# Kernel optimization log

Measured on AMD Instinct MI355X. Metric: run time of the kernel, lower is better.

## Reference

```python
import jax, jax.numpy as jnp
import numpy as np

N, E, FD, PD, C0, C1 = 50000, 1000000, 1024, 64, 64, 64


def setup_inputs() -> dict:
    key = jax.random.key(0)
    ks = iter(jax.random.split(key, 64))
    nrm = lambda s, sc=0.05: jax.random.normal(next(ks), s, jnp.float32) * sc

    def bn_p(c):
        # rows: gamma, beta, running_mean, running_var (eval-mode batchnorm)
        return jnp.stack([
            1.0 + 0.1 * jax.random.normal(next(ks), (c,)),
            0.1 * jax.random.normal(next(ks), (c,)),
            0.1 * jax.random.normal(next(ks), (c,)),
            0.5 + jax.random.uniform(next(ks), (c,)),
        ]).astype(jnp.float32)

    inp = {}
    inp["x"] = jax.random.normal(next(ks), (N, FD + 4), jnp.float32)
    inp["edge_index"] = jax.random.randint(next(ks), (2, E), 0, N, jnp.int32)
    inp["edge_attr"] = jax.random.randint(next(ks), (E,), 0, 3, jnp.int32) - 1  # {-1,0,1}
    inp["Wspf"] = nrm((PD, 4)); inp["bspf"] = nrm((PD,))
    inp["W011"] = nrm((C0, FD // 2 + PD)); inp["b011"] = nrm((C0,))
    inp["W012"] = nrm((C0, FD // 2)); inp["b012"] = nrm((C0,))
    inp["bn01"] = bn_p(C0)
    for i in (1, 2, 3):
        inp[f"e{i}W1"] = nrm((C0, 2 * C0)); inp[f"e{i}b1"] = nrm((C0,))
        inp[f"e{i}W2"] = nrm((C0, C0)); inp[f"e{i}b2"] = nrm((C0,))
        inp[f"bn1{i}"] = bn_p(C0)
    inp["s21Wl"] = nrm((C1, C0)); inp["s21bl"] = nrm((C1,)); inp["s21Wr"] = nrm((C1, C0))
    inp["bn21"] = bn_p(C1)
    for i in (1, 2, 3):
        inp[f"s3{i}Wl"] = nrm((1, C1)); inp[f"s3{i}bl"] = nrm((1,)); inp[f"s3{i}Wr"] = nrm((1, C1))
    return inp


def _bn(h, p):
    g, b, m, v = p
    return (h - m) * jax.lax.rsqrt(v + 1e-5) * g + b


def _edge_conv(h, src, dst, seg, n, W1, b1, W2, b2):
    # EdgeConv: max_j MLP([x_i, x_j - x_i]); masked edges routed to dummy segment n
    xi, xj = h[dst], h[src]
    msg = jax.nn.relu(jnp.concatenate([xi, xj - xi], axis=1) @ W1.T + b1) @ W2.T + b2
    out = jax.ops.segment_max(msg, seg, num_segments=n + 1)[:n]
    return jnp.where(jnp.isfinite(out), out, 0.0)  # nodes with no in-edges -> 0


def _sage(h, src, seg, n, Wl, bl, Wr):
    # SAGEConv: lin_l(mean_j x_j) + lin_r(x_i)
    s = jax.ops.segment_sum(h[src], seg, num_segments=n + 1)[:n]
    cnt = jax.ops.segment_sum(jnp.ones((seg.shape[0],), h.dtype), seg, num_segments=n + 1)[:n]
    agg = s / jnp.maximum(cnt, 1.0)[:, None]
    return agg @ Wl.T + bl + h @ Wr.T


def reference(x, edge_index, edge_attr, Wspf, bspf, W011, b011, W012, b012, bn01,
              e1W1, e1b1, e1W2, e1b2, bn11, e2W1, e2b1, e2W2, e2b2, bn12,
              e3W1, e3b1, e3W2, e3b2, bn13, s21Wl, s21bl, s21Wr, bn21,
              s31Wl, s31bl, s31Wr, s32Wl, s32bl, s32Wr, s33Wl, s33bl, s33Wr):
    fd = 1024
    n = x.shape[0]
    src, dst = edge_index[0], edge_index[1]
    seg1 = jnp.where(edge_attr >= 0, dst, n)  # forward-time edges
    seg2 = jnp.where(edge_attr <= 0, dst, n)  # backward-time edges
    seg3 = dst                                 # all edges

    spf = x[:, fd:fd + 4]
    x_vis = jnp.concatenate([x[:, fd // 2:fd], spf @ Wspf.T + bspf], axis=1) @ W011.T + b011
    x_aud = x[:, :fd // 2] @ W012.T + b012
    h = jax.nn.relu(_bn(x_aud + x_vis, bn01))

    def branch(eW1, eb1, eW2, eb2, bnE, seg, sWl, sbl, sWr):
        y = jax.nn.relu(_bn(_edge_conv(h, src, dst, seg, n, eW1, eb1, eW2, eb2), bnE))
        y = jax.nn.relu(_bn(_sage(y, src, seg, n, s21Wl, s21bl, s21Wr), bn21))
        return _sage(y, src, seg, n, sWl, sbl, sWr)

    o = (branch(e1W1, e1b1, e1W2, e1b2, bn11, seg1, s31Wl, s31bl, s31Wr)
         + branch(e2W1, e2b1, e2W2, e2b2, bn12, seg2, s32Wl, s32bl, s32Wr)
         + branch(e3W1, e3b1, e3W2, e3b2, bn13, seg3, s33Wl, s33bl, s33Wr))
    return jax.nn.sigmoid(o)
```

## Files before the change

kernel.cpp:

```cpp
#include <hip/hip_runtime.h>
#include <cstdint>
#include <cstddef>

#define NN 50000
#define EE 1000000
#define NBK 196
#define PW_EC 6144
#define PW_AG 8192

typedef __attribute__((ext_vector_type(8))) short bf16x8;
typedef __attribute__((ext_vector_type(4))) short s16x4;
typedef __attribute__((ext_vector_type(4))) float f32x4;
typedef _Float16 f16;
typedef __attribute__((ext_vector_type(2))) _Float16 f16x2;
typedef __attribute__((ext_vector_type(4))) _Float16 f16x4;
typedef __attribute__((ext_vector_type(8))) _Float16 f16x8;

__device__ __forceinline__ void split2(float v, short& hi, short& lo) {
    union { float f; unsigned int u; } a; a.f = v;
    unsigned short h16 = (unsigned short)(a.u >> 16);
    union { unsigned int u; float f; } hf; hf.u = ((unsigned int)h16) << 16;
    union { float f; unsigned int u; } b; b.f = v - hf.f;
    hi = (short)h16;
    lo = (short)(b.u >> 16);
}

__device__ __forceinline__ f16x8 relupq(f16x8 p, f16x8 q) {
    f16x8 s = p + q;
    f16x8 z = {};
#if __has_builtin(__builtin_elementwise_max)
    return __builtin_elementwise_max(s, z);
#else
    f16x8 r;
#pragma unroll
    for (int j = 0; j < 8; j++) r[j] = (s[j] > (f16)0.f) ? s[j] : (f16)0.f;
    return r;
#endif
}

#define OFF_WHL    ((size_t)0)
#define OFF_WSPP   ((size_t)262144)
#define OFF_BIAS01 ((size_t)263168)
#define OFF_W1PQT  ((size_t)263424)
#define OFF_BIASPQ ((size_t)361728)
#define OFF_WSAGET ((size_t)363264)
#define OFF_BIAS21 ((size_t)396032)
#define OFF_BNF    ((size_t)396288)
#define OFF_W2BF   ((size_t)398848)
#define OFF_INVC4  ((size_t)423424)
#define OFF_PZ4    ((size_t)1223424)
#define OFF_RP     ((size_t)2023424)
#define OFF_PARTS  ((size_t)2223488)
#define OFF_DEG    ((size_t)2227584)
#define OFF_GHEAD  ((size_t)2427648)
#define OFF_SORT   ((size_t)2431744)
#define OFF_H      ((size_t)6431744)
#define OFF_PI     ((size_t)19231744)
#define OFF_QI     ((size_t)38431744)
#define OFF_Y1I    ((size_t)57631744)
#define OFF_EBUCK  OFF_H
#define OFF_AGGI   OFF_PI

__global__ __launch_bounds__(256) void k_prep(
    const float* __restrict__ Wspf, const float* __restrict__ bspf,
    const float* __restrict__ W011, const float* __restrict__ b011,
    const float* __restrict__ W012, const float* __restrict__ b012,
    const float* __restrict__ bn01,
    const float* __restrict__ e1W1, const float* __restrict__ e1b1,
    const float* __restrict__ e1b2, const float* __restrict__ bn11,
    const float* __restrict__ e2W1, const float* __restrict__ e2b1,
    const float* __restrict__ e2b2, const float* __restrict__ bn12,
    const float* __restrict__ e3W1, const float* __restrict__ e3b1,
    const float* __restrict__ e3b2, const float* __restrict__ bn13,
    const float* __restrict__ e1W2, const float* __restrict__ e2W2,
    const float* __restrict__ e3W2,
    const float* __restrict__ s21Wl, const float* __restrict__ s21bl,
    const float* __restrict__ s21Wr, const float* __restrict__ bn21,
    unsigned short* __restrict__ Whl, float* __restrict__ WspP, float* __restrict__ bias01,
    float* __restrict__ W1pqT, float* __restrict__ biasPQ,
    float* __restrict__ WsageT, float* __restrict__ bias21, float* __restrict__ bnf,
    f16* __restrict__ W2h)
{
    int idx = blockIdx.x * 256 + threadIdx.x;
    if (idx < 131072) {
        int hl = idx >> 16;
        int r = idx & 65535;
        int kchunk = r >> 11;
        int r2 = r & 2047;
        int blk = r2 >> 9;
        int r3 = r2 & 511;
        int lane = r3 >> 3;
        int j = r3 & 7;
        int n = lane & 15, quad = lane >> 4;
        int k = kchunk * 32 + quad * 8 + j;
        int c = blk * 16 + n;
        float s = bn01[c] * rsqrtf(bn01[192 + c] + 1e-5f);
        float w = ((k < 512) ? W012[c * 512 + k] : W011[c * 576 + (k - 512)]) * s;
        short hi, lo;
        split2(w, hi, lo);
        Whl[idx] = (unsigned short)(hl ? lo : hi);
    } else if (idx < 131072 + 24576) {
        int r = idx - 131072;
        int b = r >> 13; r &= 8191;
        int k = r >> 7, cp = r & 127;
        const float* W1 = (b == 0) ? e1W1 : (b == 1) ? e2W1 : e3W1;
        float val;
        if (cp < 64) val = W1[cp * 128 + k] - W1[cp * 128 + 64 + k];
        else         val = W1[(cp - 64) * 128 + 64 + k];
        W1pqT[b * 8192 + k * 128 + cp] = val;
    } else if (idx < 131072 + 24576 + 8192) {
        int r = idx - (131072 + 24576);
        int k = r >> 6, c = r & 63;
        float s = bn21[c] * rsqrtf(bn21[192 + c] + 1e-5f);
        float w = (k < 64) ? s21Wl[c * 64 + k] : s21Wr[c * 64 + (k - 64)];
        WsageT[k * 64 + c] = w * s;
    } else if (idx < 131072 + 24576 + 8192 + 64) {
        int c = idx - (131072 + 24576 + 8192);
        float s01 = bn01[c] * rsqrtf(bn01[192 + c] + 1e-5f);
        float wsp0 = 0.f, wsp1 = 0.f, wsp2 = 0.f, wsp3 = 0.f, bacc = 0.f;
        for (int j = 0; j < 64; j++) {
            float w = W011[c * 576 + 512 + j];
            wsp0 += w * Wspf[j * 4 + 0];
            wsp1 += w * Wspf[j * 4 + 1];
            wsp2 += w * Wspf[j * 4 + 2];
            wsp3 += w * Wspf[j * 4 + 3];
            bacc += w * bspf[j];
        }
        WspP[c * 4 + 0] = wsp0 * s01; WspP[c * 4 + 1] = wsp1 * s01;
        WspP[c * 4 + 2] = wsp2 * s01; WspP[c * 4 + 3] = wsp3 * s01;
        bias01[c] = (b011[c] + b012[c] + bacc) * s01 + (bn01[64 + c] - bn01[128 + c] * s01);
        float s21 = bn21[c] * rsqrtf(bn21[192 + c] + 1e-5f);
        bias21[c] = s21bl[c] * s21 + (bn21[64 + c] - bn21[128 + c] * s21);
        const float* b1a[3] = { e1b1, e2b1, e3b1 };
        const float* b2a[3] = { e1b2, e2b2, e3b2 };
        const float* bna[3] = { bn11, bn12, bn13 };
#pragma unroll
        for (int b = 0; b < 3; b++) {
            float s = bna[b][c] * rsqrtf(bna[b][192 + c] + 1e-5f);
            float tr = bna[b][64 + c] - bna[b][128 + c] * s;
            bnf[b * 192 + c] = s;
            bnf[b * 192 + 64 + c] = b2a[b][c] * s + tr;
            bnf[b * 192 + 128 + c] = tr;
            biasPQ[b * 128 + c] = b1a[b][c];
            biasPQ[b * 128 + 64 + c] = 0.f;
        }
    } else if (idx < 131072 + 24576 + 8192 + 64 + 12288) {
        int r = idx - (131072 + 24576 + 8192 + 64);
        int b = r >> 12, i = r & 4095;
        const float* W2 = (b == 0) ? e1W2 : (b == 1) ? e2W2 : e3W2;
        W2h[b * 4096 + i] = (f16)W2[i];
    }
}

__global__ __launch_bounds__(256) void k_hist(
    const int* __restrict__ dst, int* __restrict__ deg)
{
    int e = blockIdx.x * 256 + threadIdx.x;
    if (e < EE) atomicAdd(&deg[dst[e]], 1);
}

__global__ __launch_bounds__(256) void k_psum(const int* __restrict__ deg, int* __restrict__ parts)
{
    int i = blockIdx.x * 256 + threadIdx.x;
    int v = (i < NN) ? deg[i] : 0;
#pragma unroll
    for (int off = 32; off > 0; off >>= 1) v += __shfl_xor(v, off);
    __shared__ int ws4[4];
    int wid = threadIdx.x >> 6;
    if ((threadIdx.x & 63) == 0) ws4[wid] = v;
    __syncthreads();
    if (threadIdx.x == 0)
        parts[blockIdx.x] = ws4[0] + ws4[1] + ws4[2] + ws4[3];
}

__global__ __launch_bounds__(256) void k_pscan(int* __restrict__ parts, int* __restrict__ ghead)
{
    __shared__ int sbuf[256];
    int tid = threadIdx.x;
    int v = (tid < NBK) ? parts[tid] : 0;
    sbuf[tid] = v;
    __syncthreads();
    for (int off = 1; off < 256; off <<= 1) {
        int t = (tid >= off) ? sbuf[tid - off] : 0;
        __syncthreads();
        sbuf[tid] += t;
        __syncthreads();
    }
    if (tid < NBK) {
        int ex = sbuf[tid] - v;
        parts[tid] = ex;
        ghead[tid] = ex;
    }
}

__global__ __launch_bounds__(256) void k_scanfix(
    const int* __restrict__ deg, const int* __restrict__ parts, int* __restrict__ rowptr)
{
    __shared__ int sbuf[256];
    int tid = threadIdx.x;
    int i = blockIdx.x * 256 + tid;
    int v = (i < NN) ? deg[i] : 0;
    sbuf[tid] = v;
    __syncthreads();
    for (int off = 1; off < 256; off <<= 1) {
        int t = (tid >= off) ? sbuf[tid - off] : 0;
        __syncthreads();
        sbuf[tid] += t;
        __syncthreads();
    }
    int base = parts[blockIdx.x];
    if (i < NN)      rowptr[i] = base + sbuf[tid] - v;
    if (i == NN - 1) rowptr[NN] = base + sbuf[tid];
}

__global__ __launch_bounds__(256) void k_bucketA(
    const int* __restrict__ src, const int* __restrict__ dst, const int* __restrict__ attr,
    int* __restrict__ ghead, unsigned int* __restrict__ ebuck)
{
    __shared__ int hist[NBK];
    __shared__ int head[NBK];
    int tid = threadIdx.x;
    if (tid < NBK) hist[tid] = 0;
    __syncthreads();
    int base_e = blockIdx.x * 4096;
    unsigned int word[16]; int bkt[16];
#pragma unroll
    for (int k = 0; k < 16; k++) {
        int e = base_e + k * 256 + tid;
        if (e < EE) {
            int d = dst[e], s = src[e], a = attr[e] + 1;
            int b = d >> 8;
            word[k] = (unsigned)s | ((unsigned)a << 16) | ((unsigned)(d & 255) << 18);
            bkt[k] = b;
            atomicAdd(&hist[b], 1);
        } else { bkt[k] = -1; word[k] = 0; }
    }
    __syncthreads();
    if (tid < NBK) {
        int c = hist[tid];
        head[tid] = c ? atomicAdd(&ghead[tid], c) : 0;
    }
    __syncthreads();
#pragma unroll
    for (int k = 0; k < 16; k++) {
        if (bkt[k] >= 0) {
            int pos = atomicAdd(&head[bkt[k]], 1);
            ebuck[pos] = word[k];
        }
    }
}

__global__ __launch_bounds__(256) void k_bucketB(
    const int* __restrict__ rp, const unsigned int* __restrict__ ebuck,
    int* __restrict__ sorted)
{
    __shared__ int sbuf[256];
    __shared__ int head[256];
    int b = blockIdx.x, tid = threadIdx.x;
    int n0 = b * 256;
    int n1 = n0 + 256; if (n1 > NN) n1 = NN;
    int r0 = rp[n0];
    int r1 = rp[n1];
    sbuf[tid] = 0;
    __syncthreads();
    for (int e = r0 + tid; e < r1; e += 256)
        atomicAdd(&sbuf[(ebuck[e] >> 18) & 255], 1);
    __syncthreads();
    int v = sbuf[tid];
    for (int off = 1; off < 256; off <<= 1) {
        int t = (tid >= off) ? sbuf[tid - off] : 0;
        __syncthreads();
        sbuf[tid] += t;
        __syncthreads();
    }
    head[tid] = r0 + sbuf[tid] - v;
    __syncthreads();
    for (int e = r0 + tid; e < r1; e += 256) {
        unsigned int w = ebuck[e];
        int pos = atomicAdd(&head[(w >> 18) & 255], 1);
        sorted[pos] = (int)(w & 0x3FFFFu);
    }
}

__global__ __launch_bounds__(256) void k_h(
    const float* __restrict__ x, const unsigned short* __restrict__ Whl,
    const float* __restrict__ WspP, const float* __restrict__ bias01,
    float* __restrict__ h)
{
    __shared__ unsigned short hib[2][4096];
    __shared__ unsigned short lob[2][4096];
    int tid = threadIdx.x;
    int w = tid >> 6, l = tid & 63;
    int tile = blockIdx.x;
    int m = l & 15, quad = l >> 4;
    int blk = w;
    const unsigned short* Wh = Whl;
    const unsigned short* Wl = Whl + 65536;
    const size_t xbase = (size_t)tile * 16 * 1028;

    int oct_w = l >> 1, off_w = (l & 1) * 4;

    f32x4 g[4];
#pragma unroll
    for (int p = 0; p < 4; p++)
        g[p] = *(const f32x4*)(x + xbase + (size_t)(p * 4 + w) * 1028 + l * 4);
#pragma unroll
    for (int p = 0; p < 4; p++) {
        int r = p * 4 + w;
        int op = r * 256 + (oct_w ^ (r & 7)) * 8 + off_w;
        s16x4 h4, l4;
#pragma unroll
        for (int i = 0; i < 4; i++) { short hi, lo; split2(g[p][i], hi, lo); h4[i] = hi; l4[i] = lo; }
        *(s16x4*)(&hib[0][op]) = h4;
        *(s16x4*)(&lob[0][op]) = l4;
    }
    __syncthreads();

    f32x4 acc = { 0.f, 0.f, 0.f, 0.f };
    for (int c = 0; c < 4; c++) {
        if (c < 3) {
#pragma unroll
            for (int p = 0; p < 4; p++)
                g[p] = *(const f32x4*)(x + xbase + (size_t)(p * 4 + w) * 1028 + (c + 1) * 256 + l * 4);
        }
        int buf = c & 1;
        const unsigned short* hp = &hib[buf][m * 256];
        const unsigned short* lp = &lob[buf][m * 256];
        int msw = m & 7;
#pragma unroll
        for (int ks = 0; ks < 8; ks++) {
            int oct = ks * 4 + quad;
            int ao = (oct ^ msw) * 8;
            bf16x8 xh = *(const bf16x8*)(hp + ao);
            bf16x8 xl = *(const bf16x8*)(lp + ao);
            int fb = (c * 8 + ks) * 2048 + blk * 512 + l * 8;
            bf16x8 bh = *(const bf16x8*)(Wh + fb);
            bf16x8 bl = *(const bf16x8*)(Wl + fb);
            acc = __builtin_amdgcn_mfma_f32_16x16x32_bf16(xh, bh, acc, 0, 0, 0);
            acc = __builtin_amdgcn_mfma_f32_16x16x32_bf16(xl, bh, acc, 0, 0, 0);
            acc = __builtin_amdgcn_mfma_f32_16x16x32_bf16(xh, bl, acc, 0, 0, 0);
        }
        if (c < 3) {
            int nbuf = (c + 1) & 1;
#pragma unroll
            for (int p = 0; p < 4; p++) {
                int r = p * 4 + w;
                int op = r * 256 + (oct_w ^ (r & 7)) * 8 + off_w;
                s16x4 h4, l4;
#pragma unroll
                for (int i = 0; i < 4; i++) { short hi, lo; split2(g[p][i], hi, lo); h4[i] = hi; l4[i] = lo; }
                *(s16x4*)(&hib[nbuf][op]) = h4;
                *(s16x4*)(&lob[nbuf][op]) = l4;
            }
            __syncthreads();
        }
    }

    int ch = blk * 16 + m;
    f32x4 wsp = *(const f32x4*)(WspP + ch * 4);
    float bia = bias01[ch];
#pragma unroll
    for (int r = 0; r < 4; r++) {
        int row = tile * 16 + quad * 4 + r;
        f32x4 sp = *(const f32x4*)(x + (size_t)row * 1028 + 1024);
        float a = acc[r] + sp[0] * wsp[0] + sp[1] * wsp[1]
                + sp[2] * wsp[2] + sp[3] * wsp[3] + bia;
        h[(size_t)row * 64 + ch] = fmaxf(a, 0.f);
    }
}

__global__ __launch_bounds__(256) void k_pq(
    const float* __restrict__ h, const float* __restrict__ WT3,
    const float* __restrict__ biasPQ, f16* __restrict__ Pi, f16* __restrict__ Qi)
{
    __shared__ float wt[64 * 128];
    __shared__ float xt[64 * 68];
    int tid = threadIdx.x;
    int m0 = blockIdx.x * 64;
    int cg = tid & 31, rg = tid >> 5;
#pragma unroll
    for (int i = 0; i < 4; i++) {
        int li = i * 256 + tid;
        int rr = li >> 4, q = li & 15;
        int row = m0 + rr;
        float4 u = make_float4(0.f, 0.f, 0.f, 0.f);
        if (row < NN) u = *(const float4*)(h + (size_t)row * 64 + q * 4);
        *(float4*)(xt + rr * 68 + q * 4) = u;
    }
    for (int b = 0; b < 3; b++) {
        __syncthreads();
#pragma unroll
        for (int i = 0; i < 8; i++)
            ((float4*)wt)[i * 256 + tid] = ((const float4*)(WT3 + b * 8192))[i * 256 + tid];
        __syncthreads();
        float acc[8][4];
#pragma unroll
        for (int r = 0; r < 8; r++)
#pragma unroll
            for (int j = 0; j < 4; j++) acc[r][j] = 0.f;
#pragma unroll 8
        for (int k = 0; k < 64; k++) {
            float4 wv = *(const float4*)(wt + k * 128 + cg * 4);
#pragma unroll
            for (int r = 0; r < 8; r++) {
                float xv = xt[(rg * 8 + r) * 68 + k];
                acc[r][0] += xv * wv.x; acc[r][1] += xv * wv.y;
                acc[r][2] += xv * wv.z; acc[r][3] += xv * wv.w;
            }
        }
        const float* biasP = biasPQ + b * 128;
#pragma unroll
        for (int r = 0; r < 8; r++) {
            int row = m0 + rg * 8 + r;
            if (row < NN) {
                if (cg < 16) {
                    f16x4 res;
#pragma unroll
                    for (int j = 0; j < 4; j++)
                        res[j] = (f16)(acc[r][j] + biasP[cg * 4 + j]);
                    *(f16x4*)(Pi + (size_t)row * 192 + b * 64 + cg * 4) = res;
                } else {
                    f16x4 res;
#pragma unroll
                    for (int j = 0; j < 4; j++)
                        res[j] = (f16)acc[r][j];
                    *(f16x4*)(Qi + (size_t)row * 192 + b * 64 + (cg - 16) * 4) = res;
                }
            }
        }
    }
}

#define ECV_LDS_BRANCH(B, PL, PH, Q0, Q1, MASK, ACC)                               \
    if ((MASK) & 0xFFFFull) {                                                      \
        f16x8 a0 = relupq(PL, Q0);                                                 \
        f16x8 a1 = relupq(PH, Q1);                                                 \
        _Pragma("unroll") for (int blk = 0; blk < 4; blk++) {                      \
            f32x4 c = { 0.f, 0.f, 0.f, 0.f };                                      \
            f16x8 w0 = *(const f16x8*)(w2s + ((B) * 8 + blk * 2 + 0) * 512 + quad * 128 + m * 8); \
            f16x8 w1 = *(const f16x8*)(w2s + ((B) * 8 + blk * 2 + 1) * 512 + quad * 128 + m * 8); \
            c = __builtin_amdgcn_mfma_f32_16x16x32_f16(a0, w0, c, 0, 0, 0);        \
            c = __builtin_amdgcn_mfma_f32_16x16x32_f16(a1, w1, c, 0, 0, 0);        \
            _Pragma("unroll") for (int r = 0; r < 4; r++)                          \
                if (((MASK) >> (vsh + r)) & 1)                                     \
                    ACC[blk][r] = fmaxf(ACC[blk][r], c[r]);                        \
        }                                                                          \
    }

#define ECV_EPI(B, ACC, CNT)                                                       \
    {                                                                              \
        float red[4];                                                              \
        _Pragma("unroll") for (int blk = 0; blk < 4; blk++) {                      \
            float rv = fmaxf(fmaxf(ACC[blk][0], ACC[blk][1]),                      \
                             fmaxf(ACC[blk][2], ACC[blk][3]));                     \
            rv = fmaxf(rv, __shfl_xor(rv, 16));                                    \
            rv = fmaxf(rv, __shfl_xor(rv, 32));                                    \
            red[blk] = rv;                                                         \
        }                                                                          \
        float mx = red[quad];                                                      \
        const float* scb = bnf + (B) * 192;                                        \
        float outv = ((CNT) > 0) ? fmaxf(fmaf(mx, scb[lane], scb[64 + lane]), 0.f) \
                                 : fmaxf(scb[128 + lane], 0.f);                    \
        y1i[(size_t)v * 192 + (B) * 64 + lane] = (f16)outv;                        \
    }

__global__ __launch_bounds__(256) void k_edgeconv_f(
    const int* __restrict__ rowptr, const int* __restrict__ sorted,
    const f16* __restrict__ Pi, const f16* __restrict__ Qi,
    const f16* __restrict__ W2h,
    const float* __restrict__ bnf,
    f16* __restrict__ y1i, float* __restrict__ invc4)
{
    __shared__ f16 w2s[12288];
    int tid = threadIdx.x;
#pragma unroll
    for (int u0 = 0; u0 < 6; u0++) {
        int u = u0 * 256 + tid;
        int frag = u >> 6;
        int rem = u & 63;
        int m2 = rem >> 2, qd = rem & 3;
        int bb = frag >> 3, blk = (frag >> 1) & 3, kc = frag & 1;
        *(int4*)(w2s + frag * 512 + qd * 128 + m2 * 8) =
            *(const int4*)(W2h + (bb * 64 + blk * 16 + m2) * 64 + kc * 32 + qd * 8);
    }
    __syncthreads();

    int wid = tid >> 6, lane = tid & 63;
    int m = lane & 15, quad = lane >> 4;
    int gw = blockIdx.x * 4 + wid;

    for (int v = gw; v < NN; v += PW_EC) {
        const f16* pr = Pi + (size_t)v * 192;
        f16x8 pl0 = *(const f16x8*)(pr + 0   + quad * 8);
        f16x8 ph0 = *(const f16x8*)(pr + 32  + quad * 8);
        f16x8 pl1 = *(const f16x8*)(pr + 64  + quad * 8);
        f16x8 ph1 = *(const f16x8*)(pr + 96  + quad * 8);
        f16x8 pl2 = *(const f16x8*)(pr + 128 + quad * 8);
        f16x8 ph2 = *(const f16x8*)(pr + 160 + quad * 8);

        int e0 = rowptr[v], e1 = rowptr[v + 1];
        int deg = e1 - e0;
        float acc0[4][4], acc1[4][4], acc2[4][4];
#pragma unroll
        for (int blk = 0; blk < 4; blk++)
#pragma unroll
            for (int r = 0; r < 4; r++) {
                acc0[blk][r] = -3.0e38f; acc1[blk][r] = -3.0e38f; acc2[blk][r] = -3.0e38f;
            }

        int cnt1 = 0, cnt2 = 0;
        int vsh = quad * 4;
        int nb = (deg + 15) >> 4;
        bool hastail = (deg & 15) != 0;
        for (int bi = 0; bi < nb; bi++) {
            bool tailb = hastail && (bi == nb - 1);
            int e = e0 + bi * 16 + m;
            bool inn = tailb ? (e < e1) : true;
            int wrd = inn ? sorted[e] : 0;
            int srcm = inn ? (wrd & 0xFFFF) : v;
            int a = (wrd >> 16) & 3;
            bool mm1 = inn && (a >= 1);
            bool mm2 = inn && (a <= 1);
            const f16* qr = Qi + (size_t)srcm * 192;
            f16x8 q30 = *(const f16x8*)(qr + 128 + quad * 8);
            f16x8 q31 = *(const f16x8*)(qr + 160 + quad * 8);
            f16x8 q10 = {}, q11 = {}, q20 = {}, q21 = {};
            if (mm1) { q10 = *(const f16x8*)(qr + quad * 8);      q11 = *(const f16x8*)(qr + 32 + quad * 8); }
            if (mm2) { q20 = *(const f16x8*)(qr + 64 + quad * 8); q21 = *(const f16x8*)(qr + 96 + quad * 8); }
            unsigned long long bl1 = __ballot(mm1);
            unsigned long long bl2 = __ballot(mm2);
            cnt1 += __popc((unsigned)bl1 & 0xFFFFu);
            cnt2 += __popc((unsigned)bl2 & 0xFFFFu);

            {
                f16x8 a30 = relupq(pl2, q30);
                f16x8 a31 = relupq(ph2, q31);
                if (!tailb) {
#pragma unroll
                    for (int blk = 0; blk < 4; blk++) {
                        f32x4 c = { 0.f, 0.f, 0.f, 0.f };
                        f16x8 w0 = *(const f16x8*)(w2s + (16 + blk * 2 + 0) * 512 + quad * 128 + m * 8);
                        f16x8 w1 = *(const f16x8*)(w2s + (16 + blk * 2 + 1) * 512 + quad * 128 + m * 8);
                        c = __builtin_amdgcn_mfma_f32_16x16x32_f16(a30, w0, c, 0, 0, 0);
                        c = __builtin_amdgcn_mfma_f32_16x16x32_f16(a31, w1, c, 0, 0, 0);
#pragma unroll
                        for (int r = 0; r < 4; r++)
                            acc2[blk][r] = fmaxf(acc2[blk][r], c[r]);
                    }
                } else {
                    unsigned long long bl3 = __ballot(inn);
#pragma unroll
                    for (int blk = 0; blk < 4; blk++) {
                        f32x4 c = { 0.f, 0.f, 0.f, 0.f };
                        f16x8 w0 = *(const f16x8*)(w2s + (16 + blk * 2 + 0) * 512 + quad * 128 + m * 8);
                        f16x8 w1 = *(const f16x8*)(w2s + (16 + blk * 2 + 1) * 512 + quad * 128 + m * 8);
                        c = __builtin_amdgcn_mfma_f32_16x16x32_f16(a30, w0, c, 0, 0, 0);
                        c = __builtin_amdgcn_mfma_f32_16x16x32_f16(a31, w1, c, 0, 0, 0);
#pragma unroll
                        for (int r = 0; r < 4; r++)
                            if ((bl3 >> (vsh + r)) & 1)
                                acc2[blk][r] = fmaxf(acc2[blk][r], c[r]);
                    }
                }
            }
            ECV_LDS_BRANCH(0, pl0, ph0, q10, q11, bl1, acc0)
            ECV_LDS_BRANCH(1, pl1, ph1, q20, q21, bl2, acc1)
        }

        ECV_EPI(0, acc0, cnt1)
        ECV_EPI(1, acc1, cnt2)
        ECV_EPI(2, acc2, deg)
        if (lane == 0) {
            float4 ic;
            ic.x = 1.f / (float)(cnt1 > 0 ? cnt1 : 1);
            ic.y = 1.f / (float)(cnt2 > 0 ? cnt2 : 1);
            ic.z = 1.f / (float)(deg  > 0 ? deg  : 1);
            ic.w = 0.f;
            *(float4*)(invc4 + (size_t)v * 4) = ic;
        }
    }
}

__global__ __launch_bounds__(256) void k_agg_f(
    const int* __restrict__ rowptr, const int* __restrict__ sorted,
    const f16* __restrict__ y1i, const float* __restrict__ invc4,
    f16* __restrict__ aggi)
{
    int wid = threadIdx.x >> 6, lane = threadIdx.x & 63;
    int eslot = lane >> 3, cg = lane & 7;
    int gw = blockIdx.x * 4 + wid;
    for (int v = gw; v < NN; v += PW_AG) {
        int e0 = rowptr[v], e1 = rowptr[v + 1];
        float s1[8], s2[8], s3[8];
#pragma unroll
        for (int j = 0; j < 8; j++) { s1[j] = 0.f; s2[j] = 0.f; s3[j] = 0.f; }
        for (int eb = e0; eb < e1; eb += 8) {
            int e = eb + eslot;
            if (e < e1) {
                int w = sorted[e];
                int src = w & 0xFFFF, a = (w >> 16) & 3;
                const f16* row = y1i + (size_t)src * 192 + cg * 8;
                f16x8 u3 = *(const f16x8*)(row + 128);
#pragma unroll
                for (int j = 0; j < 8; j++) s3[j] += (float)u3[j];
                if (a >= 1) {
                    f16x8 u1 = *(const f16x8*)(row);
#pragma unroll
                    for (int j = 0; j < 8; j++) s1[j] += (float)u1[j];
                }
                if (a <= 1) {
                    f16x8 u2 = *(const f16x8*)(row + 64);
#pragma unroll
                    for (int j = 0; j < 8; j++) s2[j] += (float)u2[j];
                }
            }
        }
#pragma unroll
        for (int j = 0; j < 8; j++) {
            s1[j] += __shfl_xor(s1[j], 8);  s1[j] += __shfl_xor(s1[j], 16); s1[j] += __shfl_xor(s1[j], 32);
            s2[j] += __shfl_xor(s2[j], 8);  s2[j] += __shfl_xor(s2[j], 16); s2[j] += __shfl_xor(s2[j], 32);
            s3[j] += __shfl_xor(s3[j], 8);  s3[j] += __shfl_xor(s3[j], 16); s3[j] += __shfl_xor(s3[j], 32);
        }
        if (eslot == 0) {
            float4 icv = *(const float4*)(invc4 + (size_t)v * 4);
            f16* od = aggi + (size_t)v * 192 + cg * 8;
            f16x8 r1, r2, r3;
#pragma unroll
            for (int j = 0; j < 8; j++) {
                r1[j] = (f16)(s1[j] * icv.x);
                r2[j] = (f16)(s2[j] * icv.y);
                r3[j] = (f16)(s3[j] * icv.z);
            }
            *(f16x8*)(od)       = r1;
            *(f16x8*)(od + 64)  = r2;
            *(f16x8*)(od + 128) = r3;
        }
    }
}

__global__ __launch_bounds__(256) void k_sage1(
    const f16* __restrict__ aggi, const f16* __restrict__ y1i,
    const float* __restrict__ WsageT, const float* __restrict__ bias21,
    const float* __restrict__ Wl0, const float* __restrict__ bl0, const float* __restrict__ Wr0,
    const float* __restrict__ Wl1, const float* __restrict__ bl1, const float* __restrict__ Wr1,
    const float* __restrict__ Wl2, const float* __restrict__ bl2, const float* __restrict__ Wr2,
    float* __restrict__ pz4)
{
    __shared__ float wt[64 * 64];
    __shared__ float xt[128 * 68];
    __shared__ float wl[64], wr[64];
    int tid = threadIdx.x;
    int m0 = blockIdx.x * 128;
    int cg = tid & 15, rg = tid >> 4;
    float zsum[8];
#pragma unroll
    for (int r = 0; r < 8; r++) zsum[r] = 0.f;

    for (int b = 0; b < 3; b++) {
        const float* Wl3 = (b == 0) ? Wl0 : (b == 1) ? Wl1 : Wl2;
        const float* bl3 = (b == 0) ? bl0 : (b == 1) ? bl1 : bl2;
        const float* Wr3 = (b == 0) ? Wr0 : (b == 1) ? Wr1 : Wr2;
        __syncthreads();
        if (tid < 64) { wl[tid] = Wl3[tid]; wr[tid] = Wr3[tid]; }
        float blv = bl3[0];
        float acc[8][4];
#pragma unroll
        for (int r = 0; r < 8; r++)
#pragma unroll
            for (int j = 0; j < 4; j++) acc[r][j] = 0.f;
        for (int ch = 0; ch < 2; ch++) {
            const f16* A = (ch ? y1i : aggi) + b * 64;
            __syncthreads();
#pragma unroll
            for (int i = 0; i < 4; i++)
                ((float4*)wt)[i * 256 + tid] = ((const float4*)(WsageT + ch * 4096))[i * 256 + tid];
#pragma unroll
            for (int i = 0; i < 4; i++) {
                int li = i * 256 + tid;
                int rr = li >> 3, q = li & 7;
                int row = m0 + rr;
                f16x8 u = {};
                if (row < NN) u = *(const f16x8*)(A + (size_t)row * 192 + q * 8);
                float4 lo4 = make_float4((float)u[0], (float)u[1], (float)u[2], (float)u[3]);
                float4 hi4 = make_float4((float)u[4], (float)u[5], (float)u[6], (float)u[7]);
                *(float4*)(xt + rr * 68 + q * 8) = lo4;
                *(float4*)(xt + rr * 68 + q * 8 + 4) = hi4;
            }
            __syncthreads();
#pragma unroll 8
            for (int k = 0; k < 64; k++) {
                float4 wv = *(const float4*)(wt + k * 64 + cg * 4);
#pragma unroll
                for (int r = 0; r < 8; r++) {
                    float xv = xt[(rg * 8 + r) * 68 + k];
                    acc[r][0] += xv * wv.x; acc[r][1] += xv * wv.y;
                    acc[r][2] += xv * wv.z; acc[r][3] += xv * wv.w;
                }
            }
        }
#pragma unroll
        for (int r = 0; r < 8; r++) {
            int row = m0 + rg * 8 + r;
            float ap = 0.f, az = 0.f;
#pragma unroll
            for (int j = 0; j < 4; j++) {
                float t = fmaxf(acc[r][j] + bias21[cg * 4 + j], 0.f);
                ap += t * wl[cg * 4 + j];
                az += t * wr[cg * 4 + j];
            }
            ap += __shfl_xor(ap, 1); ap += __shfl_xor(ap, 2);
            ap += __shfl_xor(ap, 4); ap += __shfl_xor(ap, 8);
            az += __shfl_xor(az, 1); az += __shfl_xor(az, 2);
            az += __shfl_xor(az, 4); az += __shfl_xor(az, 8);
            zsum[r] += az + blv;
            if (cg == 0 && row < NN)
                pz4[(size_t)row * 4 + b] = ap;
        }
    }
#pragma unroll
    for (int r = 0; r < 8; r++) {
        int row = m0 + rg * 8 + r;
        if (cg == 0 && row < NN)
            pz4[(size_t)row * 4 + 3] = zsum[r];
    }
}

__global__ __launch_bounds__(256) void k_sage2_f(
    const int* __restrict__ rowptr, const int* __restrict__ sorted,
    const float* __restrict__ pz4, const float* __restrict__ invc4,
    float* __restrict__ outp)
{
    int wid = threadIdx.x >> 6, lane = threadIdx.x & 63;
    int gw = blockIdx.x * 4 + wid;
    for (int v = gw; v < NN; v += PW_AG) {
        int e0 = rowptr[v], e1 = rowptr[v + 1];
        float s1 = 0.f, s2 = 0.f, s3 = 0.f;
        for (int e = e0 + lane; e < e1; e += 64) {
            int w = sorted[e];
            int src = w & 0xFFFF, a = (w >> 16) & 3;
            float4 pz = *(const float4*)(pz4 + (size_t)src * 4);
            s3 += pz.z;
            if (a >= 1) s1 += pz.x;
            if (a <= 1) s2 += pz.y;
        }
#pragma unroll
        for (int off = 32; off > 0; off >>= 1) {
            s1 += __shfl_xor(s1, off);
            s2 += __shfl_xor(s2, off);
            s3 += __shfl_xor(s3, off);
        }
        if (lane == 0) {
            float4 icv = *(const float4*)(invc4 + (size_t)v * 4);
            float zsum = pz4[(size_t)v * 4 + 3];
            float val = s1 * icv.x + s2 * icv.y + s3 * icv.z + zsum;
            outp[v] = 1.f / (1.f + expf(-val));
        }
    }
}

extern "C" void kernel_launch(void* const* d_in, const int* in_sizes, int n_in,
                              void* d_out, int out_size, void* d_ws, size_t ws_size,
                              hipStream_t stream)
{
    const float* x    = (const float*)d_in[0];
    const int* ei     = (const int*)d_in[1];
    const int* attr   = (const int*)d_in[2];
    const float* Wspf = (const float*)d_in[3];
    const float* bspf = (const float*)d_in[4];
    const float* W011 = (const float*)d_in[5];
    const float* b011 = (const float*)d_in[6];
    const float* W012 = (const float*)d_in[7];
    const float* b012 = (const float*)d_in[8];
    const float* bn01 = (const float*)d_in[9];
    const float* eW1[3] = { (const float*)d_in[10], (const float*)d_in[15], (const float*)d_in[20] };
    const float* eb1[3] = { (const float*)d_in[11], (const float*)d_in[16], (const float*)d_in[21] };
    const float* eW2[3] = { (const float*)d_in[12], (const float*)d_in[17], (const float*)d_in[22] };
    const float* eb2[3] = { (const float*)d_in[13], (const float*)d_in[18], (const float*)d_in[23] };
    const float* bn1[3] = { (const float*)d_in[14], (const float*)d_in[19], (const float*)d_in[24] };
    const float* s21Wl = (const float*)d_in[25];
    const float* s21bl = (const float*)d_in[26];
    const float* s21Wr = (const float*)d_in[27];
    const float* bn21  = (const float*)d_in[28];
    const float* s3Wl[3] = { (const float*)d_in[29], (const float*)d_in[32], (const float*)d_in[35] };
    const float* s3bl[3] = { (const float*)d_in[30], (const float*)d_in[33], (const float*)d_in[36] };
    const float* s3Wr[3] = { (const float*)d_in[31], (const float*)d_in[34], (const float*)d_in[37] };

    char* ws = (char*)d_ws;
    unsigned short* Whl = (unsigned short*)(ws + OFF_WHL);
    float* WspP   = (float*)(ws + OFF_WSPP);
    float* bias01 = (float*)(ws + OFF_BIAS01);
    float* W1pqT  = (float*)(ws + OFF_W1PQT);
    float* biasPQ = (float*)(ws + OFF_BIASPQ);
    float* WsageT = (float*)(ws + OFF_WSAGET);
    float* bias21 = (float*)(ws + OFF_BIAS21);
    float* bnf    = (float*)(ws + OFF_BNF);
    f16*   W2h    = (f16*)(ws + OFF_W2BF);
    float* invc4  = (float*)(ws + OFF_INVC4);
    float* pz4    = (float*)(ws + OFF_PZ4);
    int*   rp     = (int*)(ws + OFF_RP);
    int*   parts  = (int*)(ws + OFF_PARTS);
    int*   deg    = (int*)(ws + OFF_DEG);
    int*   ghead  = (int*)(ws + OFF_GHEAD);
    int*   sorted = (int*)(ws + OFF_SORT);
    unsigned int* ebuck = (unsigned int*)(ws + OFF_EBUCK);
    float* h      = (float*)(ws + OFF_H);
    f16*   Pi     = (f16*)(ws + OFF_PI);
    f16*   Qi     = (f16*)(ws + OFF_QI);
    f16*   y1i    = (f16*)(ws + OFF_Y1I);
    f16*   aggi   = (f16*)(ws + OFF_AGGI);

    hipMemsetAsync(ws + OFF_DEG, 0, 200064, stream);

    k_prep<<<689, 256, 0, stream>>>(
        Wspf, bspf, W011, b011, W012, b012, bn01,
        eW1[0], eb1[0], eb2[0], bn1[0],
        eW1[1], eb1[1], eb2[1], bn1[1],
        eW1[2], eb1[2], eb2[2], bn1[2],
        eW2[0], eW2[1], eW2[2],
        s21Wl, s21bl, s21Wr, bn21,
        Whl, WspP, bias01, W1pqT, biasPQ, WsageT, bias21, bnf, W2h);

    k_hist<<<3907, 256, 0, stream>>>(ei + EE, deg);
    k_psum<<<NBK, 256, 0, stream>>>(deg, parts);
    k_pscan<<<1, 256, 0, stream>>>(parts, ghead);
    k_scanfix<<<NBK, 256, 0, stream>>>(deg, parts, rp);
    k_bucketA<<<245, 256, 0, stream>>>(ei, ei + EE, attr, ghead, ebuck);
    k_bucketB<<<NBK, 256, 0, stream>>>(rp, ebuck, sorted);

    k_h<<<3125, 256, 0, stream>>>(x, Whl, WspP, bias01, h);

    k_pq<<<782, 256, 0, stream>>>(h, W1pqT, biasPQ, Pi, Qi);

    k_edgeconv_f<<<PW_EC / 4, 256, 0, stream>>>(rp, sorted, Pi, Qi, W2h, bnf, y1i, invc4);
    k_agg_f<<<PW_AG / 4, 256, 0, stream>>>(rp, sorted, y1i, invc4, aggi);

    k_sage1<<<391, 256, 0, stream>>>(aggi, y1i, WsageT, bias21,
                                     s3Wl[0], s3bl[0], s3Wr[0],
                                     s3Wl[1], s3bl[1], s3Wr[1],
                                     s3Wl[2], s3bl[2], s3Wr[2], pz4);

    k_sage2_f<<<PW_AG / 4, 256, 0, stream>>>(rp, sorted, pz4, invc4, (float*)d_out);
}
```

Before: 757.9 us.

## Sort edges by attr within each node so branches process contiguous subranges

Extends the secondary bucket sort key to include the edge attribute, so each node's edge list is grouped by attr value. It also counts per-node attr=-1 and attr=0 edges in the histogram pass. Edgeconv and aggregation then walk each branch over its own contiguous subrange, so there are no masked-out MFMAs or per-edge branch tests. The cost is three separate passes over edges, one per branch instead of one shared pass, which means more index reads and Q row gathers split across the branches. It also adds extra atomics in the histogram and a larger LDS scan in bucketB.

Measured after the change: 778.5 us. 2.7% more time.

```diff
diff --git a/kernel.cpp b/kernel.cpp
--- a/kernel.cpp
+++ b/kernel.cpp
@@ -52,12 +52,13 @@
 #define OFF_RP     ((size_t)2023424)
 #define OFF_PARTS  ((size_t)2223488)
 #define OFF_DEG    ((size_t)2227584)
-#define OFF_GHEAD  ((size_t)2427648)
-#define OFF_SORT   ((size_t)2431744)
-#define OFF_H      ((size_t)6431744)
-#define OFF_PI     ((size_t)19231744)
-#define OFF_QI     ((size_t)38431744)
-#define OFF_Y1I    ((size_t)57631744)
+#define OFF_CNT01  ((size_t)2427648)
+#define OFF_GHEAD  ((size_t)2627712)
+#define OFF_SORT   ((size_t)2631808)
+#define OFF_H      ((size_t)6631808)
+#define OFF_PI     ((size_t)19431808)
+#define OFF_QI     ((size_t)38631808)
+#define OFF_Y1I    ((size_t)57831808)
 #define OFF_EBUCK  OFF_H
 #define OFF_AGGI   OFF_PI
 
@@ -153,10 +154,17 @@
 }
 
 __global__ __launch_bounds__(256) void k_hist(
-    const int* __restrict__ dst, int* __restrict__ deg)
+    const int* __restrict__ dst, const int* __restrict__ attr,
+    int* __restrict__ deg, unsigned int* __restrict__ cnt01)
 {
     int e = blockIdx.x * 256 + threadIdx.x;
-    if (e < EE) atomicAdd(&deg[dst[e]], 1);
+    if (e < EE) {
+        int d = dst[e];
+        int a = attr[e] + 1;
+        atomicAdd(&deg[d], 1);
+        if (a == 0)      atomicAdd(&cnt01[d], 1u);
+        else if (a == 1) atomicAdd(&cnt01[d], 0x10000u);
+    }
 }
 
 __global__ __launch_bounds__(256) void k_psum(const int* __restrict__ deg, int* __restrict__ parts)
@@ -254,30 +262,39 @@
     const int* __restrict__ rp, const unsigned int* __restrict__ ebuck,
     int* __restrict__ sorted)
 {
-    __shared__ int sbuf[256];
-    __shared__ int head[256];
+    __shared__ int sbuf[1024];
+    __shared__ int head[1024];
+    __shared__ int s2[256];
     int b = blockIdx.x, tid = threadIdx.x;
     int n0 = b * 256;
     int n1 = n0 + 256; if (n1 > NN) n1 = NN;
     int r0 = rp[n0];
     int r1 = rp[n1];
-    sbuf[tid] = 0;
+    for (int i = tid; i < 1024; i += 256) sbuf[i] = 0;
     __syncthreads();
     for (int e = r0 + tid; e < r1; e += 256)
-        atomicAdd(&sbuf[(ebuck[e] >> 18) & 255], 1);
-    __syncthreads();
-    int v = sbuf[tid];
+        atomicAdd(&sbuf[(ebuck[e] >> 16) & 1023], 1);
+    __syncthreads();
+    int i0 = tid * 4;
+    int v0 = sbuf[i0], v1 = sbuf[i0 + 1], v2 = sbuf[i0 + 2], v3 = sbuf[i0 + 3];
+    int tot = v0 + v1 + v2 + v3;
+    s2[tid] = tot;
+    __syncthreads();
     for (int off = 1; off < 256; off <<= 1) {
-        int t = (tid >= off) ? sbuf[tid - off] : 0;
+        int t = (tid >= off) ? s2[tid - off] : 0;
         __syncthreads();
-        sbuf[tid] += t;
+        s2[tid] += t;
         __syncthreads();
     }
-    head[tid] = r0 + sbuf[tid] - v;
+    int ex = s2[tid] - tot;
+    head[i0]     = r0 + ex;
+    head[i0 + 1] = r0 + ex + v0;
+    head[i0 + 2] = r0 + ex + v0 + v1;
+    head[i0 + 3] = r0 + ex + v0 + v1 + v2;
     __syncthreads();
     for (int e = r0 + tid; e < r1; e += 256) {
         unsigned int w = ebuck[e];
-        int pos = atomicAdd(&head[(w >> 18) & 255], 1);
+        int pos = atomicAdd(&head[(w >> 16) & 1023], 1);
         sorted[pos] = (int)(w & 0x3FFFFu);
     }
 }
@@ -431,41 +448,69 @@
     }
 }
 
-#define ECV_LDS_BRANCH(B, PL, PH, Q0, Q1, MASK, ACC)                               \
-    if ((MASK) & 0xFFFFull) {                                                      \
-        f16x8 a0 = relupq(PL, Q0);                                                 \
-        f16x8 a1 = relupq(PH, Q1);                                                 \
-        _Pragma("unroll") for (int blk = 0; blk < 4; blk++) {                      \
-            f32x4 c = { 0.f, 0.f, 0.f, 0.f };                                      \
-            f16x8 w0 = *(const f16x8*)(w2s + ((B) * 8 + blk * 2 + 0) * 512 + quad * 128 + m * 8); \
-            f16x8 w1 = *(const f16x8*)(w2s + ((B) * 8 + blk * 2 + 1) * 512 + quad * 128 + m * 8); \
-            c = __builtin_amdgcn_mfma_f32_16x16x32_f16(a0, w0, c, 0, 0, 0);        \
-            c = __builtin_amdgcn_mfma_f32_16x16x32_f16(a1, w1, c, 0, 0, 0);        \
-            _Pragma("unroll") for (int r = 0; r < 4; r++)                          \
-                if (((MASK) >> (vsh + r)) & 1)                                     \
-                    ACC[blk][r] = fmaxf(ACC[blk][r], c[r]);                        \
+#define ECV_BRANCH(B, EST, ECN)                                                    \
+    {                                                                              \
+        f16x8 pl = *(const f16x8*)(pr + (B) * 64 + quad * 8);                      \
+        f16x8 ph = *(const f16x8*)(pr + (B) * 64 + 32 + quad * 8);                 \
+        float acc[4][4];                                                           \
+        _Pragma("unroll") for (int blk = 0; blk < 4; blk++)                        \
+            _Pragma("unroll") for (int r = 0; r < 4; r++) acc[blk][r] = -3.0e38f;  \
+        int nbF = (ECN) >> 4;                                                      \
+        int rem = (ECN) & 15;                                                      \
+        for (int bi = 0; bi < nbF; bi++) {                                         \
+            int srcm = sorted[(EST) + bi * 16 + m] & 0xFFFF;                       \
+            const f16* qr = Qi + (size_t)srcm * 192 + (B) * 64;                    \
+            f16x8 q0 = *(const f16x8*)(qr + quad * 8);                             \
+            f16x8 q1 = *(const f16x8*)(qr + 32 + quad * 8);                        \
+            f16x8 a0 = relupq(pl, q0);                                             \
+            f16x8 a1 = relupq(ph, q1);                                             \
+            _Pragma("unroll") for (int blk = 0; blk < 4; blk++) {                  \
+                f32x4 c = { 0.f, 0.f, 0.f, 0.f };                                  \
+                f16x8 w0 = *(const f16x8*)(w2s + ((B) * 8 + blk * 2 + 0) * 512 + quad * 128 + m * 8); \
+                f16x8 w1 = *(const f16x8*)(w2s + ((B) * 8 + blk * 2 + 1) * 512 + quad * 128 + m * 8); \
+                c = __builtin_amdgcn_mfma_f32_16x16x32_f16(a0, w0, c, 0, 0, 0);    \
+                c = __builtin_amdgcn_mfma_f32_16x16x32_f16(a1, w1, c, 0, 0, 0);    \
+                _Pragma("unroll") for (int r = 0; r < 4; r++)                      \
+                    acc[blk][r] = fmaxf(acc[blk][r], c[r]);                        \
+            }                                                                      \
         }                                                                          \
-    }
-
-#define ECV_EPI(B, ACC, CNT)                                                       \
-    {                                                                              \
+        if (rem) {                                                                 \
+            int e = (EST) + nbF * 16 + m;                                          \
+            int srcm = sorted[(m < rem) ? e : (EST)] & 0xFFFF;                     \
+            const f16* qr = Qi + (size_t)srcm * 192 + (B) * 64;                    \
+            f16x8 q0 = *(const f16x8*)(qr + quad * 8);                             \
+            f16x8 q1 = *(const f16x8*)(qr + 32 + quad * 8);                        \
+            f16x8 a0 = relupq(pl, q0);                                             \
+            f16x8 a1 = relupq(ph, q1);                                             \
+            _Pragma("unroll") for (int blk = 0; blk < 4; blk++) {                  \
+                f32x4 c = { 0.f, 0.f, 0.f, 0.f };                                  \
+                f16x8 w0 = *(const f16x8*)(w2s + ((B) * 8 + blk * 2 + 0) * 512 + quad * 128 + m * 8); \
+                f16x8 w1 = *(const f16x8*)(w2s + ((B) * 8 + blk * 2 + 1) * 512 + quad * 128 + m * 8); \
+                c = __builtin_amdgcn_mfma_f32_16x16x32_f16(a0, w0, c, 0, 0, 0);    \
+                c = __builtin_amdgcn_mfma_f32_16x16x32_f16(a1, w1, c, 0, 0, 0);    \
+                _Pragma("unroll") for (int r = 0; r < 4; r++)                      \
+                    if (quad * 4 + r < rem)                                        \
+                        acc[blk][r] = fmaxf(acc[blk][r], c[r]);                    \
+            }                                                                      \
+        }                                                                          \
         float red[4];                                                              \
         _Pragma("unroll") for (int blk = 0; blk < 4; blk++) {                      \
-            float rv = fmaxf(fmaxf(ACC[blk][0], ACC[blk][1]),                      \
-                             fmaxf(ACC[blk][2], ACC[blk][3]));                     \
+            float rv = fmaxf(fmaxf(acc[blk][0], acc[blk][1]),                      \
+                             fmaxf(acc[blk][2], acc[blk][3]));                     \
             rv = fmaxf(rv, __shfl_xor(rv, 16));                                    \
             rv = fmaxf(rv, __shfl_xor(rv, 32));                                    \
             red[blk] = rv;                                                         \
         }                                                                          \
         float mx = red[quad];                                                      \
         const float* scb = bnf + (B) * 192;                                        \
-        float outv = ((CNT) > 0) ? fmaxf(fmaf(mx, scb[lane], scb[64 + lane]), 0.f) \
+        float outv = ((ECN) > 0) ? fmaxf(fmaf(mx, scb[lane], scb[64 + lane]), 0.f) \
                                  : fmaxf(scb[128 + lane], 0.f);                    \
         y1i[(size_t)v * 192 + (B) * 64 + lane] = (f16)outv;                        \
     }
 
 __global__ __launch_bounds__(256) void k_edgeconv_f(
-    const int* __restrict__ rowptr, const int* __restrict__ sorted,
+    const int* __restrict__ rowptr, const unsigned int* __restrict__ cnt01,
+    const int* __restrict__ sorted,
     const f16* __restrict__ Pi, const f16* __restrict__ Qi,
     const f16* __restrict__ W2h,
     const float* __restrict__ bnf,
@@ -491,98 +536,55 @@
 
     for (int v = gw; v < NN; v += PW_EC) {
         const f16* pr = Pi + (size_t)v * 192;
-        f16x8 pl0 = *(const f16x8*)(pr + 0   + quad * 8);
-        f16x8 ph0 = *(const f16x8*)(pr + 32  + quad * 8);
-        f16x8 pl1 = *(const f16x8*)(pr + 64  + quad * 8);
-        f16x8 ph1 = *(const f16x8*)(pr + 96  + quad * 8);
-        f16x8 pl2 = *(const f16x8*)(pr + 128 + quad * 8);
-        f16x8 ph2 = *(const f16x8*)(pr + 160 + quad * 8);
-
         int e0 = rowptr[v], e1 = rowptr[v + 1];
         int deg = e1 - e0;
-        float acc0[4][4], acc1[4][4], acc2[4][4];
-#pragma unroll
-        for (int blk = 0; blk < 4; blk++)
-#pragma unroll
-            for (int r = 0; r < 4; r++) {
-                acc0[blk][r] = -3.0e38f; acc1[blk][r] = -3.0e38f; acc2[blk][r] = -3.0e38f;
-            }
-
-        int cnt1 = 0, cnt2 = 0;
-        int vsh = quad * 4;
-        int nb = (deg + 15) >> 4;
-        bool hastail = (deg & 15) != 0;
-        for (int bi = 0; bi < nb; bi++) {
-            bool tailb = hastail && (bi == nb - 1);
-            int e = e0 + bi * 16 + m;
-            bool inn = tailb ? (e < e1) : true;
-            int wrd = inn ? sorted[e] : 0;
-            int srcm = inn ? (wrd & 0xFFFF) : v;
-            int a = (wrd >> 16) & 3;
-            bool mm1 = inn && (a >= 1);
-            bool mm2 = inn && (a <= 1);
-            const f16* qr = Qi + (size_t)srcm * 192;
-            f16x8 q30 = *(const f16x8*)(qr + 128 + quad * 8);
-            f16x8 q31 = *(const f16x8*)(qr + 160 + quad * 8);
-            f16x8 q10 = {}, q11 = {}, q20 = {}, q21 = {};
-            if (mm1) { q10 = *(const f16x8*)(qr + quad * 8);      q11 = *(const f16x8*)(qr + 32 + quad * 8); }
-            if (mm2) { q20 = *(const f16x8*)(qr + 64 + quad * 8); q21 = *(const f16x8*)(qr + 96 + quad * 8); }
-            unsigned long long bl1 = __ballot(mm1);
-            unsigned long long bl2 = __ballot(mm2);
-            cnt1 += __popc((unsigned)bl1 & 0xFFFFu);
-            cnt2 += __popc((unsigned)bl2 & 0xFFFFu);
-
-            {
-                f16x8 a30 = relupq(pl2, q30);
-                f16x8 a31 = relupq(ph2, q31);
-                if (!tailb) {
-#pragma unroll
-                    for (int blk = 0; blk < 4; blk++) {
-                        f32x4 c = { 0.f, 0.f, 0.f, 0.f };
-                        f16x8 w0 = *(const f16x8*)(w2s + (16 + blk * 2 + 0) * 512 + quad * 128 + m * 8);
-                        f16x8 w1 = *(const f16x8*)(w2s + (16 + blk * 2 + 1) * 512 + quad * 128 + m * 8);
-                        c = __builtin_amdgcn_mfma_f32_16x16x32_f16(a30, w0, c, 0, 0, 0);
-                        c = __builtin_amdgcn_mfma_f32_16x16x32_f16(a31, w1, c, 0, 0, 0);
-#pragma unroll
-                        for (int r = 0; r < 4; r++)
-                            acc2[blk][r] = fmaxf(acc2[blk][r], c[r]);
-                    }
-                } else {
-                    unsigned long long bl3 = __ballot(inn);
-#pragma unroll
-                    for (int blk = 0; blk < 4; blk++) {
-                        f32x4 c = { 0.f, 0.f, 0.f, 0.f };
-                        f16x8 w0 = *(const f16x8*)(w2s + (16 + blk * 2 + 0) * 512 + quad * 128 + m * 8);
-                        f16x8 w1 = *(const f16x8*)(w2s + (16 + blk * 2 + 1) * 512 + quad * 128 + m * 8);
-                        c = __builtin_amdgcn_mfma_f32_16x16x32_f16(a30, w0, c, 0, 0, 0);
-                        c = __builtin_amdgcn_mfma_f32_16x16x32_f16(a31, w1, c, 0, 0, 0);
-#pragma unroll
-                        for (int r = 0; r < 4; r++)
-                            if ((bl3 >> (vsh + r)) & 1)
-                                acc2[blk][r] = fmaxf(acc2[blk][r], c[r]);
-                    }
-                }
-            }
-            ECV_LDS_BRANCH(0, pl0, ph0, q10, q11, bl1, acc0)
-            ECV_LDS_BRANCH(1, pl1, ph1, q20, q21, bl2, acc1)
-        }
-
-        ECV_EPI(0, acc0, cnt1)
-        ECV_EPI(1, acc1, cnt2)
-        ECV_EPI(2, acc2, deg)
+        unsigned int cc = cnt01[v];
+        int c0 = (int)(cc & 0xFFFFu);
+        int c1 = (int)(cc >> 16);
+        int n1cnt = deg - c0;
+        int n2cnt = c0 + c1;
+
+        ECV_BRANCH(0, e0 + c0, n1cnt)
+        ECV_BRANCH(1, e0, n2cnt)
+        ECV_BRANCH(2, e0, deg)
+
         if (lane == 0) {
             float4 ic;
-            ic.x = 1.f / (float)(cnt1 > 0 ? cnt1 : 1);
-            ic.y = 1.f / (float)(cnt2 > 0 ? cnt2 : 1);
-            ic.z = 1.f / (float)(deg  > 0 ? deg  : 1);
+            ic.x = 1.f / (float)(n1cnt > 0 ? n1cnt : 1);
+            ic.y = 1.f / (float)(n2cnt > 0 ? n2cnt : 1);
+            ic.z = 1.f / (float)(deg   > 0 ? deg   : 1);
             ic.w = 0.f;
             *(float4*)(invc4 + (size_t)v * 4) = ic;
         }
     }
 }
 
+#define AGG_BRANCH(B, EST, ECN, ICS)                                               \
+    {                                                                              \
+        float s[8];                                                                \
+        _Pragma("unroll") for (int j = 0; j < 8; j++) s[j] = 0.f;                  \
+        for (int eb = 0; eb < (ECN); eb += 8) {                                    \
+            if (eb + eslot < (ECN)) {                                              \
+                int src = sorted[(EST) + eb + eslot] & 0xFFFF;                     \
+                f16x8 u = *(const f16x8*)(y1i + (size_t)src * 192 + (B) * 64 + cg * 8); \
+                _Pragma("unroll") for (int j = 0; j < 8; j++) s[j] += (float)u[j]; \
+            }                                                                      \
+        }                                                                          \
+        _Pragma("unroll") for (int j = 0; j < 8; j++) {                            \
+            s[j] += __shfl_xor(s[j], 8);                                           \
+            s[j] += __shfl_xor(s[j], 16);                                          \
+            s[j] += __shfl_xor(s[j], 32);                                          \
+        }                                                                          \
+        if (eslot == 0) {                                                          \
+            f16x8 r;                                                               \
+            _Pragma("unroll") for (int j = 0; j < 8; j++) r[j] = (f16)(s[j] * (ICS)); \
+            *(f16x8*)(aggi + (size_t)v * 192 + (B) * 64 + cg * 8) = r;             \
+        }                                                                          \
+    }
+
 __global__ __launch_bounds__(256) void k_agg_f(
-    const int* __restrict__ rowptr, const int* __restrict__ sorted,
+    const int* __restrict__ rowptr, const unsigned int* __restrict__ cnt01,
+    const int* __restrict__ sorted,
     const f16* __restrict__ y1i, const float* __restrict__ invc4,
     f16* __restrict__ aggi)
 {
@@ -591,50 +593,14 @@
     int gw = blockIdx.x * 4 + wid;
     for (int v = gw; v < NN; v += PW_AG) {
         int e0 = rowptr[v], e1 = rowptr[v + 1];
-        float s1[8], s2[8], s3[8];
-#pragma unroll
-        for (int j = 0; j < 8; j++) { s1[j] = 0.f; s2[j] = 0.f; s3[j] = 0.f; }
-        for (int eb = e0; eb < e1; eb += 8) {
-            int e = eb + eslot;
-            if (e < e1) {
-                int w = sorted[e];
-                int src = w & 0xFFFF, a = (w >> 16) & 3;
-                const f16* row = y1i + (size_t)src * 192 + cg * 8;
-                f16x8 u3 = *(const f16x8*)(row + 128);
-#pragma unroll
-                for (int j = 0; j < 8; j++) s3[j] += (float)u3[j];
-                if (a >= 1) {
-                    f16x8 u1 = *(const f16x8*)(row);
-#pragma unroll
-                    for (int j = 0; j < 8; j++) s1[j] += (float)u1[j];
-                }
-                if (a <= 1) {
-                    f16x8 u2 = *(const f16x8*)(row + 64);
-#pragma unroll
-                    for (int j = 0; j < 8; j++) s2[j] += (float)u2[j];
-                }
-            }
-        }
-#pragma unroll
-        for (int j = 0; j < 8; j++) {
-            s1[j] += __shfl_xor(s1[j], 8);  s1[j] += __shfl_xor(s1[j], 16); s1[j] += __shfl_xor(s1[j], 32);
-            s2[j] += __shfl_xor(s2[j], 8);  s2[j] += __shfl_xor(s2[j], 16); s2[j] += __shfl_xor(s2[j], 32);
-            s3[j] += __shfl_xor(s3[j], 8);  s3[j] += __shfl_xor(s3[j], 16); s3[j] += __shfl_xor(s3[j], 32);
-        }
-        if (eslot == 0) {
-            float4 icv = *(const float4*)(invc4 + (size_t)v * 4);
-            f16* od = aggi + (size_t)v * 192 + cg * 8;
-            f16x8 r1, r2, r3;
-#pragma unroll
-            for (int j = 0; j < 8; j++) {
-                r1[j] = (f16)(s1[j] * icv.x);
-                r2[j] = (f16)(s2[j] * icv.y);
-                r3[j] = (f16)(s3[j] * icv.z);
-            }
-            *(f16x8*)(od)       = r1;
-            *(f16x8*)(od + 64)  = r2;
-            *(f16x8*)(od + 128) = r3;
-        }
+        int deg = e1 - e0;
+        unsigned int cc = cnt01[v];
+        int c0 = (int)(cc & 0xFFFFu);
+        int c1 = (int)(cc >> 16);
+        float4 icv = *(const float4*)(invc4 + (size_t)v * 4);
+        AGG_BRANCH(0, e0 + c0, deg - c0, icv.x)
+        AGG_BRANCH(1, e0, c0 + c1, icv.y)
+        AGG_BRANCH(2, e0, deg, icv.z)
     }
 }
 
@@ -800,6 +766,7 @@
     int*   rp     = (int*)(ws + OFF_RP);
     int*   parts  = (int*)(ws + OFF_PARTS);
     int*   deg    = (int*)(ws + OFF_DEG);
+    unsigned int* cnt01 = (unsigned int*)(ws + OFF_CNT01);
     int*   ghead  = (int*)(ws + OFF_GHEAD);
     int*   sorted = (int*)(ws + OFF_SORT);
     unsigned int* ebuck = (unsigned int*)(ws + OFF_EBUCK);
@@ -809,7 +776,7 @@
     f16*   y1i    = (f16*)(ws + OFF_Y1I);
     f16*   aggi   = (f16*)(ws + OFF_AGGI);
 
-    hipMemsetAsync(ws + OFF_DEG, 0, 200064, stream);
+    hipMemsetAsync(ws + OFF_DEG, 0, 400128, stream);
 
     k_prep<<<689, 256, 0, stream>>>(
         Wspf, bspf, W011, b011, W012, b012, bn01,
@@ -820,7 +787,7 @@
         s21Wl, s21bl, s21Wr, bn21,
         Whl, WspP, bias01, W1pqT, biasPQ, WsageT, bias21, bnf, W2h);
 
-    k_hist<<<3907, 256, 0, stream>>>(ei + EE, deg);
+    k_hist<<<3907, 256, 0, stream>>>(ei + EE, attr, deg, cnt01);
     k_psum<<<NBK, 256, 0, stream>>>(deg, parts);
     k_pscan<<<1, 256, 0, stream>>>(parts, ghead);
     k_scanfix<<<NBK, 256, 0, stream>>>(deg, parts, rp);
@@ -831,8 +798,8 @@
 
     k_pq<<<782, 256, 0, stream>>>(h, W1pqT, biasPQ, Pi, Qi);
 
-    k_edgeconv_f<<<PW_EC / 4, 256, 0, stream>>>(rp, sorted, Pi, Qi, W2h, bnf, y1i, invc4);
-    k_agg_f<<<PW_AG / 4, 256, 0, stream>>>(rp, sorted, y1i, invc4, aggi);
+    k_edgeconv_f<<<PW_EC / 4, 256, 0, stream>>>(rp, cnt01, sorted, Pi, Qi, W2h, bnf, y1i, invc4);
+    k_agg_f<<<PW_AG / 4, 256, 0, stream>>>(rp, cnt01, sorted, y1i, invc4, aggi);
 
     k_sage1<<<391, 256, 0, stream>>>(aggi, y1i, WsageT, bias21,
                                      s3Wl[0], s3bl[0], s3Wr[0],
```
